# Performance work log

Hardware: AMD Instinct MI355X
Metric: run time of the kernel (lower is better)

The kernel has to match this reference:

```python
import jax, jax.numpy as jnp
import numpy as np

EPS = 1e-7  # keras backend epsilon
ROUTINGS = 3


def squash(x, axis=-1):
    s2 = jnp.sum(jnp.square(x), axis=axis, keepdims=True)
    scale = s2 / (1.0 + s2) / jnp.sqrt(s2 + EPS)
    return scale * x


def setup_inputs() -> dict:
    key = jax.random.key(0)
    k1, k2 = jax.random.split(key)
    B, In, in_dim = 64, 2048, 16
    N, D = 32, 32
    inputs = jax.random.normal(k1, (B, In, in_dim), dtype=jnp.float32)
    W = jax.random.normal(k2, (N, In, D, in_dim), dtype=jnp.float32)  # stddev=1.0 init per module
    return {"inputs": inputs, "W": W}


def reference(inputs, W):
    # inputs: [B, In, in_dim]; W: [N, In, D, in_dim]
    # u_hat[b,n,i,d] = sum_k W[n,i,d,k] * inputs[b,i,k]
    u_hat = jnp.einsum('nidk,bik->bnid', W, inputs)  # [B, N, In, D]
    B, N, In, D = u_hat.shape
    b = jnp.zeros((B, N, In), dtype=u_hat.dtype)
    v = None
    for _ in range(ROUTINGS):
        c = jax.nn.softmax(b, axis=1)                 # softmax over output capsules
        s = jnp.einsum('bni,bnid->bnd', c, u_hat)     # weighted sum over input capsules
        v = squash(s)                                 # [B, N, D]
        b = b + jnp.einsum('bnid,bnd->bni', u_hat, v) # agreement
    return v
```

## Files before the change

### kernel.cpp

```cpp
#include <hip/hip_runtime.h>


#define INP 2048
#define BB 64
#define KK 16
#define NN 32
#define DD 32
#define ICH 16
#define NCHUNK (INP / ICH)

typedef __attribute__((ext_vector_type(8))) short short8;
typedef __attribute__((ext_vector_type(16))) float f32x16;

__device__ __forceinline__ short bf_trunc(float f) {
  return (short)(__builtin_bit_cast(unsigned, f) >> 16);
}
__device__ __forceinline__ unsigned short bf_round(float f) {
  unsigned u = __builtin_bit_cast(unsigned, f);
  return (unsigned short)((u + 0x8000u) >> 16);
}
__device__ __forceinline__ float bf2f(unsigned short u) {
  return __builtin_bit_cast(float, (unsigned)u << 16);
}

__device__ __forceinline__ void split8(float4 w0, float4 w1, short8& h, short8& l) {
  float f[8] = {w0.x, w0.y, w0.z, w0.w, w1.x, w1.y, w1.z, w1.w};
#pragma unroll
  for (int j = 0; j < 8; ++j) {
    unsigned u = __builtin_bit_cast(unsigned, f[j]);
    h[j] = (short)(u >> 16);
    float hf = __builtin_bit_cast(float, u & 0xFFFF0000u);
    l[j] = bf_trunc(f[j] - hf);
  }
}

__device__ __forceinline__ short8 round8(float4 w0, float4 w1) {
  float f[8] = {w0.x, w0.y, w0.z, w0.w, w1.x, w1.y, w1.z, w1.w};
  short8 r;
#pragma unroll
  for (int j = 0; j < 8; ++j) r[j] = (short)bf_round(f[j]);
  return r;
}

__global__ __launch_bounds__(256) void kT(const float* __restrict__ x,
                                          short* __restrict__ xh,
                                          short* __restrict__ xl) {
  const int t = blockIdx.x * 256 + threadIdx.x;
  const int i = t >> 6, b = t & 63;
  const float4* xs = (const float4*)(x + ((size_t)b * INP + i) * KK);
  short8* dh = (short8*)(xh + ((size_t)i * BB + b) * KK);
  short8* dl = (short8*)(xl + ((size_t)i * BB + b) * KK);
#pragma unroll
  for (int h = 0; h < 2; ++h) {
    short8 hh, ll;
    split8(xs[h * 2], xs[h * 2 + 1], hh, ll);
    dh[h] = hh;
    dl[h] = ll;
  }
}

__global__ __launch_bounds__(256) void kS1c(const float* __restrict__ W,
                                            const short* __restrict__ xh,
                                            const short* __restrict__ xl,
                                            short* __restrict__ Wb,
                                            unsigned short* __restrict__ spart) {
  const int wv = threadIdx.x >> 6;
  const int lane = threadIdx.x & 63;
  const int bl = lane & 31;
  const int hi = lane >> 5;
  const int w = blockIdx.x * 4 + wv;
  const int n = w >> 7;
  const int ch = w & (NCHUNK - 1);

  f32x16 s0 = {};
  f32x16 s1 = {};

  const size_t fragoff = (((size_t)n * INP + (size_t)ch * ICH) * DD + bl) * KK + hi * 8;
  const float* Wp = W + fragoff;
  short* Wbp = Wb + fragoff;
  const short* xhp = xh + (size_t)ch * ICH * BB * KK + hi * 8;
  const short* xlp = xl + (size_t)ch * ICH * BB * KK + hi * 8;

#pragma unroll 2
  for (int ii = 0; ii < ICH; ++ii) {
    float4 w0 = *(const float4*)(Wp + (size_t)ii * (DD * KK));
    float4 w1 = *(const float4*)(Wp + (size_t)ii * (DD * KK) + 4);
    short8 whi, wlo;
    split8(w0, w1, whi, wlo);
    *(short8*)(Wbp + (size_t)ii * (DD * KK)) = round8(w0, w1);
    const short8 x0h = *(const short8*)(xhp + ii * (BB * KK) + bl * KK);
    const short8 x0l = *(const short8*)(xlp + ii * (BB * KK) + bl * KK);
    const short8 x1h = *(const short8*)(xhp + ii * (BB * KK) + (bl + 32) * KK);
    const short8 x1l = *(const short8*)(xlp + ii * (BB * KK) + (bl + 32) * KK);
    s0 = __builtin_amdgcn_mfma_f32_32x32x16_bf16(whi, x0h, s0, 0, 0, 0);
    s0 = __builtin_amdgcn_mfma_f32_32x32x16_bf16(whi, x0l, s0, 0, 0, 0);
    s0 = __builtin_amdgcn_mfma_f32_32x32x16_bf16(wlo, x0h, s0, 0, 0, 0);
    s1 = __builtin_amdgcn_mfma_f32_32x32x16_bf16(whi, x1h, s1, 0, 0, 0);
    s1 = __builtin_amdgcn_mfma_f32_32x32x16_bf16(whi, x1l, s1, 0, 0, 0);
    s1 = __builtin_amdgcn_mfma_f32_32x32x16_bf16(wlo, x1h, s1, 0, 0, 0);
  }

  const size_t off = ((size_t)ch * NN + n) * (DD * BB);
#pragma unroll
  for (int r = 0; r < 16; ++r) {
    const int d = (r & 3) + 8 * (r >> 2) + 4 * hi;
    spart[off + d * BB + bl] = bf_round(0.03125f * s0[r]);
    spart[off + d * BB + bl + 32] = bf_round(0.03125f * s1[r]);
  }
}

__global__ __launch_bounds__(256) void kA(const short* __restrict__ Wb,
                                          const short* __restrict__ xh,
                                          const short* __restrict__ xl,
                                          const float* __restrict__ vsum,
                                          unsigned short* __restrict__ ct) {
  const int wv = threadIdx.x >> 6;
  const int lane = threadIdx.x & 63;
  const int bl = lane & 31;
  const int hi = lane >> 5;
  const int w = blockIdx.x * 4 + wv;
  const int n = w >> 7;
  const int ch = w & (NCHUNK - 1);

  float vr0[16], vr1[16];
#pragma unroll
  for (int r = 0; r < 16; ++r) {
    const int d = (r & 3) + 8 * (r >> 2) + 4 * hi;
    vr0[r] = vsum[((size_t)n * DD + d) * BB + bl];
    vr1[r] = vsum[((size_t)n * DD + d) * BB + bl + 32];
  }

  const short* Wp = Wb + (((size_t)n * INP + (size_t)ch * ICH) * DD + bl) * KK + hi * 8;
  const short* xhp = xh + (size_t)ch * ICH * BB * KK + hi * 8;
  const short* xlp = xl + (size_t)ch * ICH * BB * KK + hi * 8;

#pragma unroll 2
  for (int ii = 0; ii < ICH; ++ii) {
    const short8 whi = *(const short8*)(Wp + (size_t)ii * (DD * KK));
    const short8 x0h = *(const short8*)(xhp + ii * (BB * KK) + bl * KK);
    const short8 x0l = *(const short8*)(xlp + ii * (BB * KK) + bl * KK);
    const short8 x1h = *(const short8*)(xhp + ii * (BB * KK) + (bl + 32) * KK);
    const short8 x1l = *(const short8*)(xlp + ii * (BB * KK) + (bl + 32) * KK);

    f32x16 u0 = {};
    u0 = __builtin_amdgcn_mfma_f32_32x32x16_bf16(whi, x0h, u0, 0, 0, 0);
    u0 = __builtin_amdgcn_mfma_f32_32x32x16_bf16(whi, x0l, u0, 0, 0, 0);
    f32x16 u1 = {};
    u1 = __builtin_amdgcn_mfma_f32_32x32x16_bf16(whi, x1h, u1, 0, 0, 0);
    u1 = __builtin_amdgcn_mfma_f32_32x32x16_bf16(whi, x1l, u1, 0, 0, 0);

    float p0 = 0.f, p1 = 0.f;
#pragma unroll
    for (int r = 0; r < 16; ++r) {
      p0 += u0[r] * vr0[r];
      p1 += u1[r] * vr1[r];
    }
    p0 += __shfl_xor(p0, 32, 64);
    p1 += __shfl_xor(p1, 32, 64);
    const int i = ch * ICH + ii;
    ct[((size_t)i * NN + n) * BB + lane] = bf_round((lane < 32) ? p0 : p1);
  }
}

__global__ __launch_bounds__(256) void kSM(unsigned short* __restrict__ ct) {
  const int wv = threadIdx.x >> 6;
  const int lane = threadIdx.x & 63;
  const int i = blockIdx.x * 4 + wv;
  unsigned short* p = ct + (size_t)i * NN * BB + lane;
  float a[NN];
  float m = -1e30f;
#pragma unroll
  for (int n = 0; n < NN; ++n) {
    a[n] = bf2f(p[n * BB]);
    m = fmaxf(m, a[n]);
  }
  float s = 0.f;
#pragma unroll
  for (int n = 0; n < NN; ++n) {
    a[n] = __expf(a[n] - m);
    s += a[n];
  }
  const float inv = 1.f / s;
#pragma unroll
  for (int n = 0; n < NN; ++n) p[n * BB] = bf_round(a[n] * inv);
}

__global__ __launch_bounds__(256) void kS(const short* __restrict__ Wb,
                                          const short* __restrict__ xh,
                                          const short* __restrict__ xl,
                                          const unsigned short* __restrict__ ct,
                                          unsigned short* __restrict__ spart) {
  const int wv = threadIdx.x >> 6;
  const int lane = threadIdx.x & 63;
  const int bl = lane & 31;
  const int hi = lane >> 5;
  const int w = blockIdx.x * 4 + wv;
  const int n = w >> 7;
  const int ch = w & (NCHUNK - 1);

  f32x16 s0 = {};
  f32x16 s1 = {};

  const short* Wp = Wb + (((size_t)n * INP + (size_t)ch * ICH) * DD + bl) * KK + hi * 8;
  const short* xhp = xh + (size_t)ch * ICH * BB * KK + hi * 8;
  const short* xlp = xl + (size_t)ch * ICH * BB * KK + hi * 8;

#pragma unroll 2
  for (int ii = 0; ii < ICH; ++ii) {
    const short8 whi = *(const short8*)(Wp + (size_t)ii * (DD * KK));
    const short8 x0h = *(const short8*)(xhp + ii * (BB * KK) + bl * KK);
    const short8 x0l = *(const short8*)(xlp + ii * (BB * KK) + bl * KK);
    const short8 x1h = *(const short8*)(xhp + ii * (BB * KK) + (bl + 32) * KK);
    const short8 x1l = *(const short8*)(xlp + ii * (BB * KK) + (bl + 32) * KK);

    f32x16 u0 = {};
    u0 = __builtin_amdgcn_mfma_f32_32x32x16_bf16(whi, x0h, u0, 0, 0, 0);
    u0 = __builtin_amdgcn_mfma_f32_32x32x16_bf16(whi, x0l, u0, 0, 0, 0);
    f32x16 u1 = {};
    u1 = __builtin_amdgcn_mfma_f32_32x32x16_bf16(whi, x1h, u1, 0, 0, 0);
    u1 = __builtin_amdgcn_mfma_f32_32x32x16_bf16(whi, x1l, u1, 0, 0, 0);

    const int i = ch * ICH + ii;
    const float c0 = bf2f(ct[((size_t)i * NN + n) * BB + bl]);
    const float c1 = bf2f(ct[((size_t)i * NN + n) * BB + bl + 32]);
#pragma unroll
    for (int r = 0; r < 16; ++r) {
      s0[r] += c0 * u0[r];
      s1[r] += c1 * u1[r];
    }
  }

  const size_t off = ((size_t)ch * NN + n) * (DD * BB);
#pragma unroll
  for (int r = 0; r < 16; ++r) {
    const int d = (r & 3) + 8 * (r >> 2) + 4 * hi;
    spart[off + d * BB + bl] = bf_round(s0[r]);
    spart[off + d * BB + bl + 32] = bf_round(s1[r]);
  }
}

__global__ void kR1h(const unsigned* __restrict__ spart, float2* __restrict__ st) {
  const int t = blockIdx.x * 128 + threadIdx.x;
  float s0 = 0.f, s1 = 0.f;
  for (int ch = 0; ch < NCHUNK; ++ch) {
    const unsigned u = spart[(size_t)ch * (NN * DD * BB / 2) + t];
    s0 += bf2f((unsigned short)(u & 0xFFFFu));
    s1 += bf2f((unsigned short)(u >> 16));
  }
  st[t] = make_float2(s0, s1);
}

__global__ void kR2(const float* __restrict__ st, float* __restrict__ vsum,
                    float* __restrict__ out, int first, int last) {
  const int t = blockIdx.x * 256 + threadIdx.x;
  const int b = t & 63;
  const int n = t >> 6;
  float sd[DD];
  float s2 = 0.f;
#pragma unroll
  for (int d = 0; d < DD; ++d) {
    sd[d] = st[(n * DD + d) * BB + b];
    s2 += sd[d] * sd[d];
  }
  const float scale = s2 / (1.f + s2) / sqrtf(s2 + 1e-7f);
#pragma unroll
  for (int d = 0; d < DD; ++d) {
    const float v = scale * sd[d];
    const size_t idx = (size_t)(n * DD + d) * BB + b;
    vsum[idx] = first ? v : (vsum[idx] + v);
    if (last) out[((size_t)b * NN + n) * DD + d] = v;
  }
}

extern "C" void kernel_launch(void* const* d_in, const int* in_sizes, int n_in,
                              void* d_out, int out_size, void* d_ws,
                              size_t ws_size, hipStream_t stream) {
  const float* x = (const float*)d_in[0];
  const float* W = (const float*)d_in[1];
  float* out = (float*)d_out;

  short* xh = (short*)d_ws;
  short* xl = xh + (size_t)INP * BB * KK;
  short* Wbuf = xl + (size_t)INP * BB * KK;
  unsigned short* ct = (unsigned short*)(Wbuf + (size_t)NN * INP * DD * KK);
  unsigned short* sparth = ct + (size_t)INP * NN * BB;
  float* st = (float*)(sparth + (size_t)NCHUNK * NN * DD * BB);
  float* vsum = st + (size_t)NN * DD * BB;

  const int gW = (NN * NCHUNK) / 4;
  const int gT = (INP * BB) / 256;
  const int gSM = INP / 4;
  const int gR1h = (NN * DD * BB / 2) / 128;
  const int gR2 = (BB * NN) / 256;

  kT<<<gT, 256, 0, stream>>>(x, xh, xl);

  kS1c<<<gW, 256, 0, stream>>>(W, xh, xl, Wbuf, sparth);
  kR1h<<<gR1h, 128, 0, stream>>>((const unsigned*)sparth, (float2*)st);
  kR2<<<gR2, 256, 0, stream>>>(st, vsum, out, 1, 0);
  for (int it = 1; it < 3; ++it) {
    kA<<<gW, 256, 0, stream>>>(Wbuf, xh, xl, vsum, ct);
    kSM<<<gSM, 256, 0, stream>>>(ct);
    kS<<<gW, 256, 0, stream>>>(Wbuf, xh, xl, ct, sparth);
    kR1h<<<gR1h, 128, 0, stream>>>((const unsigned*)sparth, (float2*)st);
    kR2<<<gR2, 256, 0, stream>>>(st, vsum, out, 0, it == 2);
  }
}
```

Measured before the change: 185.7 us.

## Fuse agreement, softmax and weighted sum into one routing kernel

```diff
diff --git a/kernel.cpp b/kernel.cpp
--- a/kernel.cpp
+++ b/kernel.cpp
@@ -7,7 +7,9 @@
 #define NN 32
 #define DD 32
 #define ICH 16
-#define NCHUNK (INP / ICH)
+#define SCH (INP / ICH)
+#define FICH 8
+#define FNCH (INP / FICH)
 
 typedef __attribute__((ext_vector_type(8))) short short8;
 typedef __attribute__((ext_vector_type(16))) float f32x16;
@@ -33,7 +35,6 @@
     l[j] = bf_trunc(f[j] - hf);
   }
 }
-
 __device__ __forceinline__ short8 round8(float4 w0, float4 w1) {
   float f[8] = {w0.x, w0.y, w0.z, w0.w, w1.x, w1.y, w1.z, w1.w};
   short8 r;
@@ -70,7 +71,7 @@
   const int hi = lane >> 5;
   const int w = blockIdx.x * 4 + wv;
   const int n = w >> 7;
-  const int ch = w & (NCHUNK - 1);
+  const int ch = w & (SCH - 1);
 
   f32x16 s0 = {};
   f32x16 s1 = {};
@@ -109,140 +110,111 @@
   }
 }
 
-__global__ __launch_bounds__(256) void kA(const short* __restrict__ Wb,
-                                          const short* __restrict__ xh,
-                                          const short* __restrict__ xl,
-                                          const float* __restrict__ vsum,
-                                          unsigned short* __restrict__ ct) {
-  const int wv = threadIdx.x >> 6;
+__global__ __launch_bounds__(512, 4) void kF2(const short* __restrict__ Wb,
+                                              const short* __restrict__ xh,
+                                              const short* __restrict__ xl,
+                                              const float* __restrict__ vsumT,
+                                              unsigned short* __restrict__ spart) {
+  __shared__ unsigned short sm[FICH][32][NN + 2];
+  const int w = threadIdx.x >> 6;
   const int lane = threadIdx.x & 63;
   const int bl = lane & 31;
   const int hi = lane >> 5;
-  const int w = blockIdx.x * 4 + wv;
-  const int n = w >> 7;
-  const int ch = w & (NCHUNK - 1);
-
-  float vr0[16], vr1[16];
-#pragma unroll
-  for (int r = 0; r < 16; ++r) {
-    const int d = (r & 3) + 8 * (r >> 2) + 4 * hi;
-    vr0[r] = vsum[((size_t)n * DD + d) * BB + bl];
-    vr1[r] = vsum[((size_t)n * DD + d) * BB + bl + 32];
-  }
-
-  const short* Wp = Wb + (((size_t)n * INP + (size_t)ch * ICH) * DD + bl) * KK + hi * 8;
-  const short* xhp = xh + (size_t)ch * ICH * BB * KK + hi * 8;
-  const short* xlp = xl + (size_t)ch * ICH * BB * KK + hi * 8;
-
+  const int bi = blockIdx.x;
+  const int ch = bi >> 1;
+  const int bh = bi & 1;
+  const size_t i0 = (size_t)ch * FICH;
+
+  const short* xbase_h = xh + (i0 * BB + (size_t)bh * 32 + bl) * KK + hi * 8;
+  const short* xbase_l = xl + (i0 * BB + (size_t)bh * 32 + bl) * KK + hi * 8;
+
+  for (int nr = 0; nr < 4; ++nr) {
+    const int n = w * 4 + nr;
+    float vr[16];
+    const float* vp = vsumT + ((size_t)n * BB + bh * 32 + bl) * DD + hi * 4;
+#pragma unroll
+    for (int g = 0; g < 4; ++g) {
+      float4 v4 = *(const float4*)(vp + g * 8);
+      vr[g * 4 + 0] = v4.x;
+      vr[g * 4 + 1] = v4.y;
+      vr[g * 4 + 2] = v4.z;
+      vr[g * 4 + 3] = v4.w;
+    }
+    const short* Wp = Wb + (((size_t)n * INP + i0) * DD + bl) * KK + hi * 8;
 #pragma unroll 2
-  for (int ii = 0; ii < ICH; ++ii) {
-    const short8 whi = *(const short8*)(Wp + (size_t)ii * (DD * KK));
-    const short8 x0h = *(const short8*)(xhp + ii * (BB * KK) + bl * KK);
-    const short8 x0l = *(const short8*)(xlp + ii * (BB * KK) + bl * KK);
-    const short8 x1h = *(const short8*)(xhp + ii * (BB * KK) + (bl + 32) * KK);
-    const short8 x1l = *(const short8*)(xlp + ii * (BB * KK) + (bl + 32) * KK);
-
-    f32x16 u0 = {};
-    u0 = __builtin_amdgcn_mfma_f32_32x32x16_bf16(whi, x0h, u0, 0, 0, 0);
-    u0 = __builtin_amdgcn_mfma_f32_32x32x16_bf16(whi, x0l, u0, 0, 0, 0);
-    f32x16 u1 = {};
-    u1 = __builtin_amdgcn_mfma_f32_32x32x16_bf16(whi, x1h, u1, 0, 0, 0);
-    u1 = __builtin_amdgcn_mfma_f32_32x32x16_bf16(whi, x1l, u1, 0, 0, 0);
-
-    float p0 = 0.f, p1 = 0.f;
+    for (int ii = 0; ii < FICH; ++ii) {
+      const short8 wf = *(const short8*)(Wp + (size_t)ii * (DD * KK));
+      const short8 xf = *(const short8*)(xbase_h + (size_t)ii * (BB * KK));
+      f32x16 u = {};
+      u = __builtin_amdgcn_mfma_f32_32x32x16_bf16(wf, xf, u, 0, 0, 0);
+      float p = 0.f;
+#pragma unroll
+      for (int r = 0; r < 16; ++r) p += u[r] * vr[r];
+      p += __shfl_xor(p, 32, 64);
+      if (hi == 0) sm[ii][bl][n] = bf_round(p);
+    }
+  }
+  __syncthreads();
+
+  if (threadIdx.x < 256) {
+    const int ii = threadIdx.x >> 5;
+    const int b = threadIdx.x & 31;
+    unsigned* row = (unsigned*)&sm[ii][b][0];
+    float a[NN];
+    float m = -1e30f;
+#pragma unroll
+    for (int j = 0; j < 16; ++j) {
+      const unsigned u = row[j];
+      a[2 * j] = bf2f((unsigned short)(u & 0xFFFFu));
+      a[2 * j + 1] = bf2f((unsigned short)(u >> 16));
+      m = fmaxf(m, fmaxf(a[2 * j], a[2 * j + 1]));
+    }
+    float s = 0.f;
+#pragma unroll
+    for (int n = 0; n < NN; ++n) {
+      a[n] = __expf(a[n] - m);
+      s += a[n];
+    }
+    const float inv = 1.f / s;
+#pragma unroll
+    for (int j = 0; j < 16; ++j) {
+      const unsigned lo = bf_round(a[2 * j] * inv);
+      const unsigned hs = bf_round(a[2 * j + 1] * inv);
+      row[j] = lo | (hs << 16);
+    }
+  }
+  __syncthreads();
+
+  for (int nr = 0; nr < 4; ++nr) {
+    const int n = w * 4 + nr;
+    f32x16 s = {};
+    const short* Wp = Wb + (((size_t)n * INP + i0) * DD + bl) * KK + hi * 8;
+#pragma unroll 2
+    for (int ii = 0; ii < FICH; ++ii) {
+      const short8 wf = *(const short8*)(Wp + (size_t)ii * (DD * KK));
+      const short8 xfh = *(const short8*)(xbase_h + (size_t)ii * (BB * KK));
+      const short8 xfl = *(const short8*)(xbase_l + (size_t)ii * (BB * KK));
+      f32x16 u = {};
+      u = __builtin_amdgcn_mfma_f32_32x32x16_bf16(wf, xfh, u, 0, 0, 0);
+      u = __builtin_amdgcn_mfma_f32_32x32x16_bf16(wf, xfl, u, 0, 0, 0);
+      const float c = bf2f(sm[ii][bl][n]);
+#pragma unroll
+      for (int r = 0; r < 16; ++r) s[r] += c * u[r];
+    }
+    const size_t off = ((size_t)ch * NN + n) * (DD * BB) + bh * 32;
 #pragma unroll
     for (int r = 0; r < 16; ++r) {
-      p0 += u0[r] * vr0[r];
-      p1 += u1[r] * vr1[r];
-    }
-    p0 += __shfl_xor(p0, 32, 64);
-    p1 += __shfl_xor(p1, 32, 64);
-    const int i = ch * ICH + ii;
-    ct[((size_t)i * NN + n) * BB + lane] = bf_round((lane < 32) ? p0 : p1);
-  }
-}
-
-__global__ __launch_bounds__(256) void kSM(unsigned short* __restrict__ ct) {
-  const int wv = threadIdx.x >> 6;
-  const int lane = threadIdx.x & 63;
-  const int i = blockIdx.x * 4 + wv;
-  unsigned short* p = ct + (size_t)i * NN * BB + lane;
-  float a[NN];
-  float m = -1e30f;
-#pragma unroll
-  for (int n = 0; n < NN; ++n) {
-    a[n] = bf2f(p[n * BB]);
-    m = fmaxf(m, a[n]);
-  }
-  float s = 0.f;
-#pragma unroll
-  for (int n = 0; n < NN; ++n) {
-    a[n] = __expf(a[n] - m);
-    s += a[n];
-  }
-  const float inv = 1.f / s;
-#pragma unroll
-  for (int n = 0; n < NN; ++n) p[n * BB] = bf_round(a[n] * inv);
-}
-
-__global__ __launch_bounds__(256) void kS(const short* __restrict__ Wb,
-                                          const short* __restrict__ xh,
-                                          const short* __restrict__ xl,
-                                          const unsigned short* __restrict__ ct,
-                                          unsigned short* __restrict__ spart) {
-  const int wv = threadIdx.x >> 6;
-  const int lane = threadIdx.x & 63;
-  const int bl = lane & 31;
-  const int hi = lane >> 5;
-  const int w = blockIdx.x * 4 + wv;
-  const int n = w >> 7;
-  const int ch = w & (NCHUNK - 1);
-
-  f32x16 s0 = {};
-  f32x16 s1 = {};
-
-  const short* Wp = Wb + (((size_t)n * INP + (size_t)ch * ICH) * DD + bl) * KK + hi * 8;
-  const short* xhp = xh + (size_t)ch * ICH * BB * KK + hi * 8;
-  const short* xlp = xl + (size_t)ch * ICH * BB * KK + hi * 8;
-
-#pragma unroll 2
-  for (int ii = 0; ii < ICH; ++ii) {
-    const short8 whi = *(const short8*)(Wp + (size_t)ii * (DD * KK));
-    const short8 x0h = *(const short8*)(xhp + ii * (BB * KK) + bl * KK);
-    const short8 x0l = *(const short8*)(xlp + ii * (BB * KK) + bl * KK);
-    const short8 x1h = *(const short8*)(xhp + ii * (BB * KK) + (bl + 32) * KK);
-    const short8 x1l = *(const short8*)(xlp + ii * (BB * KK) + (bl + 32) * KK);
-
-    f32x16 u0 = {};
-    u0 = __builtin_amdgcn_mfma_f32_32x32x16_bf16(whi, x0h, u0, 0, 0, 0);
-    u0 = __builtin_amdgcn_mfma_f32_32x32x16_bf16(whi, x0l, u0, 0, 0, 0);
-    f32x16 u1 = {};
-    u1 = __builtin_amdgcn_mfma_f32_32x32x16_bf16(whi, x1h, u1, 0, 0, 0);
-    u1 = __builtin_amdgcn_mfma_f32_32x32x16_bf16(whi, x1l, u1, 0, 0, 0);
-
-    const int i = ch * ICH + ii;
-    const float c0 = bf2f(ct[((size_t)i * NN + n) * BB + bl]);
-    const float c1 = bf2f(ct[((size_t)i * NN + n) * BB + bl + 32]);
-#pragma unroll
-    for (int r = 0; r < 16; ++r) {
-      s0[r] += c0 * u0[r];
-      s1[r] += c1 * u1[r];
-    }
-  }
-
-  const size_t off = ((size_t)ch * NN + n) * (DD * BB);
-#pragma unroll
-  for (int r = 0; r < 16; ++r) {
-    const int d = (r & 3) + 8 * (r >> 2) + 4 * hi;
-    spart[off + d * BB + bl] = bf_round(s0[r]);
-    spart[off + d * BB + bl + 32] = bf_round(s1[r]);
-  }
-}
-
-__global__ void kR1h(const unsigned* __restrict__ spart, float2* __restrict__ st) {
+      const int d = (r & 3) + 8 * (r >> 2) + 4 * hi;
+      spart[off + d * BB + bl] = bf_round(s[r]);
+    }
+  }
+}
+
+__global__ void kR1h(const unsigned* __restrict__ spart, float2* __restrict__ st,
+                     int nch) {
   const int t = blockIdx.x * 128 + threadIdx.x;
   float s0 = 0.f, s1 = 0.f;
-  for (int ch = 0; ch < NCHUNK; ++ch) {
+  for (int ch = 0; ch < nch; ++ch) {
     const unsigned u = spart[(size_t)ch * (NN * DD * BB / 2) + t];
     s0 += bf2f((unsigned short)(u & 0xFFFFu));
     s1 += bf2f((unsigned short)(u >> 16));
@@ -250,9 +222,9 @@
   st[t] = make_float2(s0, s1);
 }
 
-__global__ void kR2(const float* __restrict__ st, float* __restrict__ vsum,
+__global__ void kR2(const float* __restrict__ st, float* __restrict__ vsumT,
                     float* __restrict__ out, int first, int last) {
-  const int t = blockIdx.x * 256 + threadIdx.x;
+  const int t = blockIdx.x * 64 + threadIdx.x;
   const int b = t & 63;
   const int n = t >> 6;
   float sd[DD];
@@ -263,11 +235,11 @@
     s2 += sd[d] * sd[d];
   }
   const float scale = s2 / (1.f + s2) / sqrtf(s2 + 1e-7f);
+  float* vp = vsumT + ((size_t)n * BB + b) * DD;
 #pragma unroll
   for (int d = 0; d < DD; ++d) {
     const float v = scale * sd[d];
-    const size_t idx = (size_t)(n * DD + d) * BB + b;
-    vsum[idx] = first ? v : (vsum[idx] + v);
+    vp[d] = first ? v : (vp[d] + v);
     if (last) out[((size_t)b * NN + n) * DD + d] = v;
   }
 }
@@ -282,27 +254,24 @@
   short* xh = (short*)d_ws;
   short* xl = xh + (size_t)INP * BB * KK;
   short* Wbuf = xl + (size_t)INP * BB * KK;
-  unsigned short* ct = (unsigned short*)(Wbuf + (size_t)NN * INP * DD * KK);
-  unsigned short* sparth = ct + (size_t)INP * NN * BB;
-  float* st = (float*)(sparth + (size_t)NCHUNK * NN * DD * BB);
-  float* vsum = st + (size_t)NN * DD * BB;
-
-  const int gW = (NN * NCHUNK) / 4;
+  unsigned short* sparth = (unsigned short*)(Wbuf + (size_t)NN * INP * DD * KK);
+  float* st = (float*)(sparth + (size_t)FNCH * NN * DD * BB);
+  float* vsumT = st + (size_t)NN * DD * BB;
+
+  const int gS = (NN * SCH) / 4;
   const int gT = (INP * BB) / 256;
-  const int gSM = INP / 4;
-  const int gR1h = (NN * DD * BB / 2) / 128;
-  const int gR2 = (BB * NN) / 256;
+  const int gF = FNCH * 2;
+  const int gR1 = (NN * DD * BB / 2) / 128;
+  const int gR2 = (BB * NN) / 64;
 
   kT<<<gT, 256, 0, stream>>>(x, xh, xl);
 
-  kS1c<<<gW, 256, 0, stream>>>(W, xh, xl, Wbuf, sparth);
-  kR1h<<<gR1h, 128, 0, stream>>>((const unsigned*)sparth, (float2*)st);
-  kR2<<<gR2, 256, 0, stream>>>(st, vsum, out, 1, 0);
+  kS1c<<<gS, 256, 0, stream>>>(W, xh, xl, Wbuf, sparth);
+  kR1h<<<gR1, 128, 0, stream>>>((const unsigned*)sparth, (float2*)st, SCH);
+  kR2<<<gR2, 64, 0, stream>>>(st, vsumT, out, 1, 0);
   for (int it = 1; it < 3; ++it) {
-    kA<<<gW, 256, 0, stream>>>(Wbuf, xh, xl, vsum, ct);
-    kSM<<<gSM, 256, 0, stream>>>(ct);
-    kS<<<gW, 256, 0, stream>>>(Wbuf, xh, xl, ct, sparth);
-    kR1h<<<gR1h, 128, 0, stream>>>((const unsigned*)sparth, (float2*)st);
-    kR2<<<gR2, 256, 0, stream>>>(st, vsum, out, 0, it == 2);
-  }
-}
+    kF2<<<gF, 512, 0, stream>>>(Wbuf, xh, xl, vsumT, sparth);
+    kR1h<<<gR1, 128, 0, stream>>>((const unsigned*)sparth, (float2*)st, FNCH);
+    kR2<<<gR2, 64, 0, stream>>>(st, vsumT, out, 0, it == 2);
+  }
+}
```

Result: slower. 344.8 us (+85.6%).
